# Performance work log

Measured on AMD Instinct MI355X. Metric: run time of the kernel, lower is better.

## Reference

```python
import jax, jax.numpy as jnp
import numpy as np

WS, OWS, NH = 16, 24, 2          # window size, overlap window size (=int(16*0.5)+16), num heads
PAD = (OWS - WS) // 2            # unfold padding = 4


def conv2d(x, w, b):
    kh, kw = w.shape[2], w.shape[3]
    out = jax.lax.conv_general_dilated(x, w, (1, 1), [(kh // 2, kh // 2), (kw // 2, kw // 2)],
                                       dimension_numbers=('NCHW', 'OIHW', 'NCHW'))
    return out + b[None, :, None, None]


def layer_norm(x, g, b, eps=1e-5):
    m = x.mean(-1, keepdims=True)
    v = ((x - m) ** 2).mean(-1, keepdims=True)
    return (x - m) * jax.lax.rsqrt(v + eps) * g + b


def stem(depth, cw1, cb1, cw2, cb2, cw3, cb3, cw4, cb4, in_g, in_b):
    # BasicConv(1->8,k3,relu) -> (8->16,k1,relu) -> (16->16,k3,relu) -> (16->32,k1) -> InstanceNorm2d(32,affine)
    y = jax.nn.relu(conv2d(depth, cw1, cb1))
    y = jax.nn.relu(conv2d(y, cw2, cb2))
    y = jax.nn.relu(conv2d(y, cw3, cb3))
    y = conv2d(y, cw4, cb4)
    m = y.mean((2, 3), keepdims=True)
    v = ((y - m) ** 2).mean((2, 3), keepdims=True)
    return (y - m) * jax.lax.rsqrt(v + 1e-5) * in_g[None, :, None, None] + in_b[None, :, None, None]


def ocab(xq, ykv, rpi, n1g, n1b, wq, bq, wkv, bkv, rpb, wp, bp, n2g, n2b, mw1, mb1, mw2, mb2):
    # Overlapping cross-attention block (HAT-style OCAB, cross variant: q from xq, kv from ykv).
    b, c, h, w = xq.shape
    x = xq.transpose(0, 2, 3, 1)   # b h w c
    y = ykv.transpose(0, 2, 3, 1)
    shortcut = x
    q = layer_norm(x, n1g, n1b) @ wq + bq          # b h w c
    kv = layer_norm(y, n1g, n1b) @ wkv + bkv       # b h w 2c
    nhw, nww = h // WS, w // WS
    # non-overlapping query windows: (b*nw, WS*WS, c)
    qw = q.reshape(b, nhw, WS, nww, WS, c).transpose(0, 1, 3, 2, 4, 5).reshape(b * nhw * nww, WS * WS, c)
    # overlapping kv windows via unfold (patch channel order = (channel, kh, kw), same as torch unfold)
    patches = jax.lax.conv_general_dilated_patches(kv.transpose(0, 3, 1, 2), (OWS, OWS), (WS, WS),
                                                   [(PAD, PAD), (PAD, PAD)])  # b, 2c*OWS*OWS, nhw, nww
    patches = patches.reshape(b, 2, c, OWS * OWS, nhw * nww).transpose(1, 0, 4, 3, 2).reshape(2, b * nhw * nww, OWS * OWS, c)
    k, v = patches[0], patches[1]
    d = c // NH
    qh = qw.reshape(-1, WS * WS, NH, d).transpose(0, 2, 1, 3) * (d ** -0.5)
    kh = k.reshape(-1, OWS * OWS, NH, d).transpose(0, 2, 1, 3)
    vh = v.reshape(-1, OWS * OWS, NH, d).transpose(0, 2, 1, 3)
    attn = jnp.einsum('whqd,whkd->whqk', qh, kh)
    attn = attn + rpb[rpi].transpose(2, 0, 1)[None]  # rel-pos bias -> [1, NH, WS*WS, OWS*OWS]
    attn = jax.nn.softmax(attn, axis=-1)
    out = jnp.einsum('whqk,whkd->whqd', attn, vh).transpose(0, 2, 1, 3).reshape(-1, WS * WS, c)
    # window reverse
    out = out.reshape(b, nhw, nww, WS, WS, c).transpose(0, 1, 3, 2, 4, 5).reshape(b, h, w, c)
    out = out @ wp + bp + shortcut
    out = out + (jax.nn.gelu(layer_norm(out, n2g, n2b) @ mw1 + mb1) @ mw2 + mb2)  # mlp_ratio=2
    return out.transpose(0, 3, 1, 2)


def setup_inputs():
    key = jax.random.key(0)
    ks = jax.random.split(key, 16)
    B, C, H, W = 1, 32, 256, 256
    s = 0.05
    return dict(
        x=jax.random.normal(ks[0], (B, C, H, W), jnp.float32),
        depth=jax.random.normal(ks[1], (B, 1, H, W), jnp.float32),
        rpi=jax.random.randint(ks[2], (WS * WS, OWS * OWS), 0, (WS + OWS - 1) ** 2),
        cw1=jax.random.normal(ks[3], (8, 1, 3, 3)) * s, cb1=jnp.zeros(8),
        cw2=jax.random.normal(ks[4], (16, 8, 1, 1)) * s, cb2=jnp.zeros(16),
        cw3=jax.random.normal(ks[5], (16, 16, 3, 3)) * s, cb3=jnp.zeros(16),
        cw4=jax.random.normal(ks[6], (32, 16, 1, 1)) * s, cb4=jnp.zeros(32),
        in_g=jnp.ones(32), in_b=jnp.zeros(32),
        n1g=jnp.ones(C), n1b=jnp.zeros(C),
        wq=jax.random.normal(ks[7], (C, C)) * s, bq=jnp.zeros(C),
        wkv=jax.random.normal(ks[8], (C, 2 * C)) * s, bkv=jnp.zeros(2 * C),
        rpb=jax.random.normal(ks[9], ((WS + OWS - 1) ** 2, NH)) * 0.02,
        wp=jax.random.normal(ks[10], (C, C)) * s, bp=jnp.zeros(C),
        n2g=jnp.ones(C), n2b=jnp.zeros(C),
        mw1=jax.random.normal(ks[11], (C, 2 * C)) * s, mb1=jnp.zeros(2 * C),
        mw2=jax.random.normal(ks[12], (2 * C, C)) * s, mb2=jnp.zeros(C),
    )


def reference(x, depth, rpi, cw1, cb1, cw2, cb2, cw3, cb3, cw4, cb4, in_g, in_b,
              n1g, n1b, wq, bq, wkv, bkv, rpb, wp, bp, n2g, n2b, mw1, mb1, mw2, mb2):
    f = stem(depth, cw1, cb1, cw2, cb2, cw3, cb3, cw4, cb4, in_g, in_b)
    a = (n1g, n1b, wq, bq, wkv, bkv, rpb, wp, bp, n2g, n2b, mw1, mb1, mw2, mb2)
    out1 = ocab(x, f, rpi, *a)   # shared OCAB weights, called twice with swapped roles
    out2 = ocab(f, x, rpi, *a)
    return out1 + out2 + x
```

## Files before the change

### kernel.cpp

```cpp
#include <hip/hip_runtime.h>
#include <hip/hip_bf16.h>

#define HW 65536
#define KPAD 584

typedef __attribute__((ext_vector_type(8))) short bf8;
typedef __attribute__((ext_vector_type(4))) float f4;

__device__ __forceinline__ unsigned short f2b(float x) {
  unsigned int u = __float_as_uint(x);
  unsigned int r = (u + 0x7fff + ((u >> 16) & 1)) >> 16;
  return (unsigned short)r;
}
__device__ __forceinline__ unsigned int pk2(float lo, float hi) {
  return (__float_as_uint(hi) & 0xffff0000u) | (__float_as_uint(lo) >> 16);
}
__device__ __forceinline__ unsigned int pkrne(float lo, float hi) {
  return ((unsigned int)f2b(hi) << 16) | (unsigned int)f2b(lo);
}
__device__ __forceinline__ float ex2(float x) { return __builtin_amdgcn_exp2f(x); }

__device__ __forceinline__ void stem_front_body(
    int bx, int t, const float* __restrict__ depth,
    const float* __restrict__ cw1, const float* __restrict__ cb1,
    const float* __restrict__ cw2, const float* __restrict__ cb2,
    float* __restrict__ t2) {
  int p = bx * 256 + t;
  int y = p >> 8, x = p & 255;
  float in9[9];
#pragma unroll
  for (int ky = 0; ky < 3; ky++)
#pragma unroll
    for (int kx = 0; kx < 3; kx++) {
      int yy = y + ky - 1, xx = x + kx - 1;
      bool ok = ((unsigned)yy < 256u) && ((unsigned)xx < 256u);
      in9[ky*3+kx] = ok ? depth[yy*256+xx] : 0.f;
    }
  float t1[8];
#pragma unroll
  for (int o = 0; o < 8; o++) {
    float s = cb1[o];
#pragma unroll
    for (int i = 0; i < 9; i++) s += in9[i] * cw1[o*9+i];
    t1[o] = fmaxf(s, 0.f);
  }
#pragma unroll
  for (int o = 0; o < 16; o++) {
    float s = cb2[o];
#pragma unroll
    for (int ci = 0; ci < 8; ci++) s += t1[ci] * cw2[o*8+ci];
    t2[o*HW + p] = fmaxf(s, 0.f);
  }
}

__device__ __forceinline__ void bias_body(
    int bx, int t, const int* __restrict__ rpi,
    const float* __restrict__ rpb, float* __restrict__ biasT) {
  int idx = bx*256 + t;
  int hd = idx / 147456;
  int rem = idx - hd*147456;
  int qt = rem / 9216;
  int r2 = rem - qt*9216;
  int kb = r2 >> 6;
  int q16 = (r2 >> 2) & 15;
  int r = r2 & 3;
  int key = kb*4 + r;
  int qq = qt*16 + q16;
  biasT[idx] = (rpb[rpi[qq*576 + key]*2 + hd] - 8.0f) * 1.44269504f;
}

__device__ __forceinline__ void lnmm48_body(
    int role, int bx, int t,
    float* ws, float* gs, float* bs, float* b2s, float* as_, float* bbs_,
    const float* __restrict__ x, const float* __restrict__ t4,
    const float* __restrict__ part,
    const float* __restrict__ ig, const float* __restrict__ ib,
    const float* __restrict__ n1g, const float* __restrict__ n1b,
    const float* __restrict__ wq, const float* __restrict__ bq,
    const float* __restrict__ wkv, const float* __restrict__ bkv,
    unsigned int* __restrict__ q1, unsigned int* __restrict__ kv1,
    unsigned int* __restrict__ q2, unsigned int* __restrict__ kv2) {
  const float QS = 0.360673503f;
  bool ain = role >= 2;
  int slice = role & 1;
  const float* src = ain ? t4 : x;
  unsigned int* dq  = ain ? q2 : q1;
  unsigned int* dkv = ain ? kv1 : kv2;
  for (int i = t; i < 1536; i += 256) {
    int c = i / 48, j = i - c*48;
    ws[i] = slice ? wkv[c*64 + 16 + j]
                  : (j < 32 ? wq[c*32 + j] : wkv[c*64 + (j - 32)]);
  }
  if (t < 48) b2s[t] = slice ? bkv[16 + t] : (t < 32 ? bq[t] : bkv[t - 32]);
  if (t < 32) {
    gs[t] = n1g[t]; bs[t] = n1b[t];
    if (ain) {
      float s = 0.f, ss = 0.f;
#pragma unroll
      for (int k = 0; k < 16; k++) { s += part[t*16+k]; ss += part[512 + t*16+k]; }
      float m = s * (1.f/65536.f);
      float var = ss * (1.f/65536.f) - m*m;
      float a = rsqrtf(var + 1e-5f) * ig[t];
      as_[t] = a; bbs_[t] = ib[t] - m*a;
    }
  }
  __syncthreads();
  int p = bx*256 + t;
  float v[32]; float s = 0.f;
  if (ain) {
#pragma unroll
    for (int c = 0; c < 32; c++) { v[c] = src[c*HW+p]*as_[c] + bbs_[c]; s += v[c]; }
  } else {
#pragma unroll
    for (int c = 0; c < 32; c++) { v[c] = src[c*HW+p]; s += v[c]; }
  }
  float m = s * 0.03125f;
  float ss = 0.f;
#pragma unroll
  for (int c = 0; c < 32; c++) { float d = v[c]-m; ss += d*d; }
  float rs = rsqrtf(ss*0.03125f + 1e-5f);
  float acc[48];
#pragma unroll
  for (int j = 0; j < 48; j++) acc[j] = b2s[j];
#pragma unroll
  for (int c = 0; c < 32; c++) {
    float ln = (v[c]-m)*rs*gs[c] + bs[c];
    const float4* w4 = (const float4*)&ws[c*48];
#pragma unroll
    for (int j4 = 0; j4 < 12; j4++) {
      float4 w = w4[j4];
      acc[j4*4+0] += ln*w.x; acc[j4*4+1] += ln*w.y;
      acc[j4*4+2] += ln*w.z; acc[j4*4+3] += ln*w.w;
    }
  }
  if (slice == 0) {
#pragma unroll
    for (int j2 = 0; j2 < 16; j2++)
      dq[j2*HW+p] = pkrne(acc[2*j2]*QS, acc[2*j2+1]*QS);
#pragma unroll
    for (int c2 = 0; c2 < 8; c2++)
      dkv[c2*HW+p] = pkrne(acc[32+2*c2], acc[32+2*c2+1]);
  } else {
#pragma unroll
    for (int c2 = 0; c2 < 24; c2++)
      dkv[(8+c2)*HW+p] = pkrne(acc[2*c2], acc[2*c2+1]);
  }
}

__global__ __launch_bounds__(256) void k_misc(
    const float* __restrict__ depth,
    const float* __restrict__ cw1, const float* __restrict__ cb1,
    const float* __restrict__ cw2, const float* __restrict__ cb2,
    float* __restrict__ t2,
    const int* __restrict__ rpi, const float* __restrict__ rpb, float* __restrict__ biasT,
    const float* __restrict__ x, const float* __restrict__ t4,
    const float* __restrict__ part,
    const float* __restrict__ ig, const float* __restrict__ ib,
    const float* __restrict__ n1g, const float* __restrict__ n1b,
    const float* __restrict__ wq, const float* __restrict__ bq,
    const float* __restrict__ wkv, const float* __restrict__ bkv,
    unsigned int* q1, unsigned int* kv1, unsigned int* q2, unsigned int* kv2) {
  __shared__ __align__(16) float ws[1536];
  __shared__ float gs[32], bs[32], b2s[48], as_[32], bbs_[32];
  int id = blockIdx.x, t = threadIdx.x;
  if (id < 256) { stem_front_body(id, t, depth, cw1, cb1, cw2, cb2, t2); return; }
  if (id < 1408) { bias_body(id - 256, t, rpi, rpb, biasT); return; }
  int r = id - 1408;
  lnmm48_body(r >> 8, r & 255, t, ws, gs, bs, b2s, as_, bbs_,
              x, t4, part, ig, ib, n1g, n1b, wq, bq, wkv, bkv, q1, kv1, q2, kv2);
}

__global__ __launch_bounds__(256) void k_lnmmB(
    const float* __restrict__ x, const float* __restrict__ t4,
    const float* __restrict__ part,
    const float* __restrict__ ig, const float* __restrict__ ib,
    const float* __restrict__ n1g, const float* __restrict__ n1b,
    const float* __restrict__ wq, const float* __restrict__ bq,
    const float* __restrict__ wkv, const float* __restrict__ bkv,
    unsigned int* q1, unsigned int* kv1, unsigned int* q2, unsigned int* kv2) {
  __shared__ __align__(16) float ws[1536];
  __shared__ float gs[32], bs[32], b2s[48], as_[32], bbs_[32];
  lnmm48_body(2 + blockIdx.y, blockIdx.x, threadIdx.x, ws, gs, bs, b2s, as_, bbs_,
              x, t4, part, ig, ib, n1g, n1b, wq, bq, wkv, bkv, q1, kv1, q2, kv2);
}

__global__ __launch_bounds__(256) void k_conv3(
    const float* __restrict__ t2, const float* __restrict__ cw3,
    const float* __restrict__ cb3, float* __restrict__ t3) {
  int t = threadIdx.x;
  int p = blockIdx.x*256 + t;
  int og = blockIdx.y;
  int y = p >> 8, x = p & 255;
  float acc[4];
#pragma unroll
  for (int o = 0; o < 4; o++) acc[o] = cb3[og*4+o];
#pragma unroll 1
  for (int tap = 0; tap < 9; tap++) {
    int ky = tap/3 - 1, kx = tap - (tap/3)*3 - 1;
    int yy = y+ky, xx = x+kx;
    bool ok = ((unsigned)yy < 256u) && ((unsigned)xx < 256u);
    int pp = yy*256+xx;
#pragma unroll
    for (int ci = 0; ci < 16; ci++) {
      float v = ok ? t2[ci*HW+pp] : 0.f;
#pragma unroll
      for (int o = 0; o < 4; o++)
        acc[o] += v * cw3[(og*4+o)*144 + ci*9 + tap];
    }
  }
#pragma unroll
  for (int o = 0; o < 4; o++) t3[(og*4+o)*HW+p] = fmaxf(acc[o], 0.f);
}

__global__ __launch_bounds__(256) void k_conv4(
    const float* __restrict__ t3, const float* __restrict__ cw4,
    const float* __restrict__ cb4, float* __restrict__ t4) {
  int t = threadIdx.x;
  int p = blockIdx.x*256 + t;
  int og = blockIdx.y;
  float v[16];
#pragma unroll
  for (int ci = 0; ci < 16; ci++) v[ci] = t3[ci*HW+p];
#pragma unroll
  for (int o = 0; o < 8; o++) {
    int oo = og*8 + o;
    float s = cb4[oo];
#pragma unroll
    for (int ci = 0; ci < 16; ci++) s += v[ci]*cw4[oo*16+ci];
    t4[oo*HW+p] = s;
  }
}

__global__ __launch_bounds__(256) void k_instats1(const float* __restrict__ t4,
                                                  float* __restrict__ part) {
  int c = blockIdx.x >> 4, seg = blockIdx.x & 15;
  const float4* src = (const float4*)(t4 + c*HW + seg*4096);
  float s = 0.f, ss = 0.f;
  for (int i = threadIdx.x; i < 1024; i += 256) {
    float4 v = src[i];
    s  += v.x + v.y + v.z + v.w;
    ss += v.x*v.x + v.y*v.y + v.z*v.z + v.w*v.w;
  }
#pragma unroll
  for (int off = 32; off > 0; off >>= 1) {
    s  += __shfl_down(s, off, 64);
    ss += __shfl_down(ss, off, 64);
  }
  __shared__ float sh[8];
  int wid = threadIdx.x >> 6;
  if ((threadIdx.x & 63) == 0) { sh[wid] = s; sh[4+wid] = ss; }
  __syncthreads();
  if (threadIdx.x == 0) {
    part[blockIdx.x]       = sh[0]+sh[1]+sh[2]+sh[3];
    part[512 + blockIdx.x] = sh[4]+sh[5]+sh[6]+sh[7];
  }
}

__global__ __launch_bounds__(256, 4) void k_attn(
    const unsigned int* __restrict__ qA, const unsigned int* __restrict__ kvA,
    float* __restrict__ aoA,
    const unsigned int* __restrict__ qB, const unsigned int* __restrict__ kvB,
    float* __restrict__ aoB,
    const float* __restrict__ biasT) {
  __shared__ __align__(16) unsigned short Ks[576*16];
  __shared__ __align__(16) unsigned short Vt[16*KPAD];

  const unsigned int* q  = blockIdx.y ? qB  : qA;
  const unsigned int* kv = blockIdx.y ? kvB : kvA;
  float* ao              = blockIdx.y ? aoB : aoA;

  int id = blockIdx.x;
  int lin = ((id & 7) << 6) | (id >> 3);
  int wi = lin >> 1, hd = lin & 1;
  int wy = wi >> 4, wx = wi & 15;
  int t = threadIdx.x;
  int by = wy*16 - 4, bx = wx*16 - 4;
  int krow = hd*8, vrow = 16 + hd*8;

  int wave = t >> 6, lane = t & 63;
  int quad = lane >> 4, l16 = lane & 15;
  const bf8 zero8 = {0,0,0,0,0,0,0,0};

  bf8 qf[4];
#pragma unroll
  for (int qi = 0; qi < 4; qi++) {
    if (quad < 2) {
      int qt = wave*4 + qi;
      int prow = (wy*16 + qt)*256 + wx*16 + l16;
      union { unsigned int u[4]; bf8 v; } Q;
#pragma unroll
      for (int jw = 0; jw < 4; jw++)
        Q.u[jw] = q[(krow + quad*4 + jw)*HW + prow];
      qf[qi] = Q.v;
    } else {
      qf[qi] = zero8;
    }
  }

  for (int e = t; e < 576; e += 256) {
    int dy = e / 24, dx = e - dy*24;
    int yy = by + dy, xx = bx + dx;
    bool ok = ((unsigned)yy < 256u) && ((unsigned)xx < 256u);
    int pp = yy*256 + xx;
    int off = e & 31;
    int ppos = ((off & 12) << 1) + ((off >> 4) << 2) + (off & 3);
    int vcol = (e & ~31) + ppos;
    unsigned int kwd[8];
#pragma unroll
    for (int i = 0; i < 8; i++) kwd[i] = ok ? kv[(krow + i)*HW + pp] : 0u;
    *(uint4*)&Ks[e*16]     = *(const uint4*)&kwd[0];
    *(uint4*)&Ks[e*16 + 8] = *(const uint4*)&kwd[4];
#pragma unroll
    for (int i = 0; i < 8; i++) {
      unsigned int vw = ok ? kv[(vrow + i)*HW + pp] : 0u;
      Vt[(2*i)*KPAD + vcol]   = (unsigned short)vw;
      Vt[(2*i+1)*KPAD + vcol] = (unsigned short)(vw >> 16);
    }
  }
  __syncthreads();

  f4 oacc[4];
  float lr[4];
  const float* bb[4];
#pragma unroll
  for (int qi = 0; qi < 4; qi++) {
    int qt = wave*4 + qi;
    oacc[qi] = (f4){0.f,0.f,0.f,0.f};
    lr[qi] = 0.f;
    bb[qi] = biasT + (hd*16 + qt)*9216 + quad*64 + l16*4;
  }

#pragma unroll 2
  for (int kt2 = 0; kt2 < 18; kt2++) {
    int k0 = kt2 * 32;
    bf8 kf0 = zero8, kf1 = zero8;
    if (quad < 2) {
      kf0 = *(const bf8*)&Ks[(k0 + l16)*16 + quad*8];
      kf1 = *(const bf8*)&Ks[(k0 + 16 + l16)*16 + quad*8];
    }
    bf8 vf = *(const bf8*)&Vt[l16*KPAD + k0 + quad*8];
    __builtin_amdgcn_s_setprio(1);
#pragma unroll
    for (int qi = 0; qi < 4; qi++) {
      f4 b0 = *(const f4*)&bb[qi][k0*16];
      f4 b1 = *(const f4*)&bb[qi][(k0+16)*16];
      f4 s0 = __builtin_amdgcn_mfma_f32_16x16x32_bf16(kf0, qf[qi], b0, 0, 0, 0);
      f4 s1 = __builtin_amdgcn_mfma_f32_16x16x32_bf16(kf1, qf[qi], b1, 0, 0, 0);
      float p0[4], p1[4];
#pragma unroll
      for (int r = 0; r < 4; r++) {
        p0[r] = ex2(s0[r]);
        p1[r] = ex2(s1[r]);
        lr[qi] += p0[r] + p1[r];
      }
      union { unsigned int u[4]; bf8 v; } P;
      P.u[0] = pk2(p0[0], p0[1]); P.u[1] = pk2(p0[2], p0[3]);
      P.u[2] = pk2(p1[0], p1[1]); P.u[3] = pk2(p1[2], p1[3]);
      oacc[qi] = __builtin_amdgcn_mfma_f32_16x16x32_bf16(P.v, vf, oacc[qi], 0, 0, 0);
    }
    __builtin_amdgcn_s_setprio(0);
  }
#pragma unroll
  for (int qi = 0; qi < 4; qi++) {
    lr[qi] += __shfl_xor(lr[qi], 16, 64);
    lr[qi] += __shfl_xor(lr[qi], 32, 64);
  }
#pragma unroll
  for (int qi = 0; qi < 4; qi++) {
    int qt = wave*4 + qi;
#pragma unroll
    for (int r = 0; r < 4; r++) {
      float lv = __shfl(lr[qi], quad*4 + r, 64);
      int qw = qt*16 + quad*4 + r;
      ao[(hd*16 + l16)*HW + (wy*16 + (qw >> 4))*256 + wx*16 + (qw & 15)] = oacc[qi][r] / lv;
    }
  }
}

__global__ __launch_bounds__(256) void k_projmlp(
    const float* __restrict__ ao1, const float* __restrict__ ao2,
    const float* __restrict__ x, const float* __restrict__ t4,
    const float* __restrict__ part,
    const float* __restrict__ ig, const float* __restrict__ ib,
    const float* __restrict__ wp, const float* __restrict__ bp,
    const float* __restrict__ n2g, const float* __restrict__ n2b,
    const float* __restrict__ mw1, const float* __restrict__ mb1,
    const float* __restrict__ mw2, const float* __restrict__ mb2,
    float* __restrict__ o1, float* __restrict__ o2, int obase) {
  int oc = blockIdx.y + obase;
  const float* ao = oc ? ao2 : ao1;
  float* dst      = oc ? o2  : o1;
  __shared__ __align__(16) float wps[1024];
  __shared__ __align__(16) float w1s[2048];
  __shared__ __align__(16) float w2s[2048];
  __shared__ float bps[32], b1s[64], b2s[32], gs[32], bs[32], as[32], bbs[32];
  int t = threadIdx.x;
  for (int i = t; i < 1024; i += 256) wps[i] = wp[i];
  for (int i = t; i < 2048; i += 256) { w1s[i] = mw1[i]; w2s[i] = mw2[i]; }
  if (t < 64) b1s[t] = mb1[t];
  if (t < 32) {
    bps[t] = bp[t]; b2s[t] = mb2[t]; gs[t] = n2g[t]; bs[t] = n2b[t];
    float s = 0.f, ss = 0.f;
#pragma unroll
    for (int k = 0; k < 16; k++) { s += part[t*16+k]; ss += part[512 + t*16+k]; }
    float m = s * (1.f/65536.f);
    float var = ss * (1.f/65536.f) - m*m;
    float a = rsqrtf(var + 1e-5f) * ig[t];
    as[t] = a; bbs[t] = ib[t] - m*a;
  }
  __syncthreads();
  int p = blockIdx.x*256 + t;
  float acc[32];
#pragma unroll
  for (int j = 0; j < 32; j++) acc[j] = bps[j];
#pragma unroll
  for (int c = 0; c < 32; c++) {
    float vc = ao[c*HW+p];
    const float4* w4 = (const float4*)&wps[c*32];
#pragma unroll
    for (int j4 = 0; j4 < 8; j4++) {
      float4 w = w4[j4];
      acc[j4*4+0] += vc*w.x; acc[j4*4+1] += vc*w.y;
      acc[j4*4+2] += vc*w.z; acc[j4*4+3] += vc*w.w;
    }
  }
  if (oc == 0) {
#pragma unroll
    for (int j = 0; j < 32; j++) acc[j] += x[j*HW+p];
  } else {
#pragma unroll
    for (int j = 0; j < 32; j++) acc[j] += t4[j*HW+p]*as[j] + bbs[j];
  }
  float s = 0.f;
#pragma unroll
  for (int j = 0; j < 32; j++) s += acc[j];
  float m = s * 0.03125f;
  float ss = 0.f;
#pragma unroll
  for (int j = 0; j < 32; j++) { float d = acc[j]-m; ss += d*d; }
  float rs = rsqrtf(ss*0.03125f + 1e-5f);
  float r[32];
#pragma unroll
  for (int j = 0; j < 32; j++) r[j] = b2s[j];
#pragma unroll 1
  for (int half = 0; half < 2; half++) {
    float h[32];
#pragma unroll
    for (int k = 0; k < 32; k++) h[k] = b1s[half*32 + k];
#pragma unroll
    for (int c = 0; c < 32; c++) {
      float ln = (acc[c] - m) * rs * gs[c] + bs[c];
      const float4* w4 = (const float4*)&w1s[c*64 + half*32];
#pragma unroll
      for (int k4 = 0; k4 < 8; k4++) {
        float4 w = w4[k4];
        h[k4*4+0] += ln*w.x; h[k4*4+1] += ln*w.y; h[k4*4+2] += ln*w.z; h[k4*4+3] += ln*w.w;
      }
    }
#pragma unroll
    for (int k = 0; k < 32; k++) {
      float xx = h[k];
      float u = 0.7978845608f * (xx + 0.044715f*xx*xx*xx);
      float th = 1.f - 2.f/(1.f + __expf(2.f*u));
      h[k] = 0.5f * xx * (1.f + th);
    }
#pragma unroll
    for (int k = 0; k < 32; k++) {
      float hk = h[k];
      const float4* w4 = (const float4*)&w2s[(half*32 + k)*32];
#pragma unroll
      for (int j4 = 0; j4 < 8; j4++) {
        float4 w = w4[j4];
        r[j4*4+0] += hk*w.x; r[j4*4+1] += hk*w.y; r[j4*4+2] += hk*w.z; r[j4*4+3] += hk*w.w;
      }
    }
  }
#pragma unroll
  for (int j = 0; j < 32; j++) dst[j*HW + p] = acc[j] + r[j];
}

__global__ __launch_bounds__(256) void k_final(
    const float* o1, const float* __restrict__ o2,
    const float* __restrict__ x, float* out) {
  int i = blockIdx.x*256 + threadIdx.x;
  float4 a = ((const float4*)o1)[i];
  float4 b = ((const float4*)o2)[i];
  float4 c = ((const float4*)x)[i];
  float4 r;
  r.x = a.x + b.x + c.x; r.y = a.y + b.y + c.y;
  r.z = a.z + b.z + c.z; r.w = a.w + b.w + c.w;
  ((float4*)out)[i] = r;
}

extern "C" void kernel_launch(void* const* d_in, const int* in_sizes, int n_in,
                              void* d_out, int out_size, void* d_ws, size_t ws_size,
                              hipStream_t stream) {
  const float* x    = (const float*)d_in[0];
  const float* depth= (const float*)d_in[1];
  const int*   rpi  = (const int*)d_in[2];
  const float* cw1  = (const float*)d_in[3],  *cb1 = (const float*)d_in[4];
  const float* cw2  = (const float*)d_in[5],  *cb2 = (const float*)d_in[6];
  const float* cw3  = (const float*)d_in[7],  *cb3 = (const float*)d_in[8];
  const float* cw4  = (const float*)d_in[9],  *cb4 = (const float*)d_in[10];
  const float* in_g = (const float*)d_in[11], *in_b = (const float*)d_in[12];
  const float* n1g  = (const float*)d_in[13], *n1b = (const float*)d_in[14];
  const float* wq   = (const float*)d_in[15], *bq  = (const float*)d_in[16];
  const float* wkv  = (const float*)d_in[17], *bkv = (const float*)d_in[18];
  const float* rpb  = (const float*)d_in[19];
  const float* wp   = (const float*)d_in[20], *bp  = (const float*)d_in[21];
  const float* n2g  = (const float*)d_in[22], *n2b = (const float*)d_in[23];
  const float* mw1  = (const float*)d_in[24], *mb1 = (const float*)d_in[25];
  const float* mw2  = (const float*)d_in[26], *mb2 = (const float*)d_in[27];

  float* W   = (float*)d_ws;
  float* o1  = (float*)d_out;

  float* t4    = W;
  unsigned int* q1  = (unsigned int*)(W + 2097152);
  unsigned int* q2  = (unsigned int*)(W + 3145728);
  unsigned int* kv1 = (unsigned int*)(W + 4194304);
  unsigned int* kv2 = (unsigned int*)(W + 6291456);
  float* ao1   = W + 8388608;
  float* ao2   = W + 10485760;
  float* biasT = W + 12582912;
  float* part  = W + 12877824;
  float* t2 = ao1;
  float* t3 = ao2;
  float* o2 = W + 2097152;

  k_misc   <<<1920, 256, 0, stream>>>(depth, cw1, cb1, cw2, cb2, t2,
                                      rpi, rpb, biasT,
                                      x, t4, part, in_g, in_b, n1g, n1b,
                                      wq, bq, wkv, bkv, q1, kv1, q2, kv2);
  k_conv3  <<<dim3(256,4), 256, 0, stream>>>(t2, cw3, cb3, t3);
  k_conv4  <<<dim3(256,4), 256, 0, stream>>>(t3, cw4, cb4, t4);
  k_instats1<<<512, 256, 0, stream>>>(t4, part);
  k_lnmmB  <<<dim3(256,2), 256, 0, stream>>>(x, t4, part, in_g, in_b, n1g, n1b,
                                             wq, bq, wkv, bkv, q1, kv1, q2, kv2);
  k_attn   <<<dim3(512,2), 256, 0, stream>>>(q1, kv1, ao1, q2, kv2, ao2, biasT);
  k_projmlp<<<dim3(256,2), 256, 0, stream>>>(ao1, ao2, x, t4, part, in_g, in_b,
                                             wp, bp, n2g, n2b, mw1, mb1, mw2, mb2,
                                             o1, o2, 0);
  k_final  <<<2048, 256, 0, stream>>>(o1, o2, x, o1);
}
```

Before: 256.0 us.

## Fuse both OCAB proj/MLP passes and final sum into one kernel; bf16 LN weights

Each thread of k_projmlp now processes both OCAB branches for its pixel at once. The two second-MLP outputs are summed directly into one accumulator and the residuals plus x are added in place, so the o2 intermediate and the k_final kernel are removed. Separately, the LN+QKV projection weights are staged in shared memory as packed bf16 and unpacked on the fly, halving their LDS footprint and load count. The costs are more registers per thread and only 256 blocks for the fused kernel, which may hurt occupancy and latency hiding, and the bf16 weights add rounding error to Q/K/V.

```diff
diff --git a/kernel.cpp b/kernel.cpp
--- a/kernel.cpp
+++ b/kernel.cpp
@@ -18,6 +18,8 @@
 __device__ __forceinline__ unsigned int pkrne(float lo, float hi) {
   return ((unsigned int)f2b(hi) << 16) | (unsigned int)f2b(lo);
 }
+__device__ __forceinline__ float blo(unsigned int u) { return __uint_as_float(u << 16); }
+__device__ __forceinline__ float bhi(unsigned int u) { return __uint_as_float(u & 0xffff0000u); }
 __device__ __forceinline__ float ex2(float x) { return __builtin_amdgcn_exp2f(x); }
 
 __device__ __forceinline__ void stem_front_body(
@@ -71,7 +73,7 @@
 
 __device__ __forceinline__ void lnmm48_body(
     int role, int bx, int t,
-    float* ws, float* gs, float* bs, float* b2s, float* as_, float* bbs_,
+    unsigned int* ws16, float* gs, float* bs, float* b2s, float* as_, float* bbs_,
     const float* __restrict__ x, const float* __restrict__ t4,
     const float* __restrict__ part,
     const float* __restrict__ ig, const float* __restrict__ ib,
@@ -86,10 +88,14 @@
   const float* src = ain ? t4 : x;
   unsigned int* dq  = ain ? q2 : q1;
   unsigned int* dkv = ain ? kv1 : kv2;
-  for (int i = t; i < 1536; i += 256) {
-    int c = i / 48, j = i - c*48;
-    ws[i] = slice ? wkv[c*64 + 16 + j]
-                  : (j < 32 ? wq[c*32 + j] : wkv[c*64 + (j - 32)]);
+  for (int i = t; i < 768; i += 256) {
+    int c = i / 24, jw = i - c*24;
+    int j = jw*2;
+    float a, b;
+    if (slice) { a = wkv[c*64 + 16 + j]; b = wkv[c*64 + 16 + j + 1]; }
+    else if (j < 32) { a = wq[c*32 + j]; b = wq[c*32 + j + 1]; }
+    else { a = wkv[c*64 + (j - 32)]; b = wkv[c*64 + (j - 31)]; }
+    ws16[i] = pkrne(a, b);
   }
   if (t < 48) b2s[t] = slice ? bkv[16 + t] : (t < 32 ? bq[t] : bkv[t - 32]);
   if (t < 32) {
@@ -125,12 +131,14 @@
 #pragma unroll
   for (int c = 0; c < 32; c++) {
     float ln = (v[c]-m)*rs*gs[c] + bs[c];
-    const float4* w4 = (const float4*)&ws[c*48];
-#pragma unroll
-    for (int j4 = 0; j4 < 12; j4++) {
-      float4 w = w4[j4];
-      acc[j4*4+0] += ln*w.x; acc[j4*4+1] += ln*w.y;
-      acc[j4*4+2] += ln*w.z; acc[j4*4+3] += ln*w.w;
+    const uint4* w4 = (const uint4*)&ws16[c*24];
+#pragma unroll
+    for (int q4 = 0; q4 < 6; q4++) {
+      uint4 w = w4[q4];
+      acc[q4*8+0] += ln*blo(w.x); acc[q4*8+1] += ln*bhi(w.x);
+      acc[q4*8+2] += ln*blo(w.y); acc[q4*8+3] += ln*bhi(w.y);
+      acc[q4*8+4] += ln*blo(w.z); acc[q4*8+5] += ln*bhi(w.z);
+      acc[q4*8+6] += ln*blo(w.w); acc[q4*8+7] += ln*bhi(w.w);
     }
   }
   if (slice == 0) {
@@ -160,13 +168,13 @@
     const float* __restrict__ wq, const float* __restrict__ bq,
     const float* __restrict__ wkv, const float* __restrict__ bkv,
     unsigned int* q1, unsigned int* kv1, unsigned int* q2, unsigned int* kv2) {
-  __shared__ __align__(16) float ws[1536];
+  __shared__ __align__(16) unsigned int ws16[768];
   __shared__ float gs[32], bs[32], b2s[48], as_[32], bbs_[32];
   int id = blockIdx.x, t = threadIdx.x;
   if (id < 256) { stem_front_body(id, t, depth, cw1, cb1, cw2, cb2, t2); return; }
   if (id < 1408) { bias_body(id - 256, t, rpi, rpb, biasT); return; }
   int r = id - 1408;
-  lnmm48_body(r >> 8, r & 255, t, ws, gs, bs, b2s, as_, bbs_,
+  lnmm48_body(r >> 8, r & 255, t, ws16, gs, bs, b2s, as_, bbs_,
               x, t4, part, ig, ib, n1g, n1b, wq, bq, wkv, bkv, q1, kv1, q2, kv2);
 }
 
@@ -178,9 +186,9 @@
     const float* __restrict__ wq, const float* __restrict__ bq,
     const float* __restrict__ wkv, const float* __restrict__ bkv,
     unsigned int* q1, unsigned int* kv1, unsigned int* q2, unsigned int* kv2) {
-  __shared__ __align__(16) float ws[1536];
+  __shared__ __align__(16) unsigned int ws16[768];
   __shared__ float gs[32], bs[32], b2s[48], as_[32], bbs_[32];
-  lnmm48_body(2 + blockIdx.y, blockIdx.x, threadIdx.x, ws, gs, bs, b2s, as_, bbs_,
+  lnmm48_body(2 + blockIdx.y, blockIdx.x, threadIdx.x, ws16, gs, bs, b2s, as_, bbs_,
               x, t4, part, ig, ib, n1g, n1b, wq, bq, wkv, bkv, q1, kv1, q2, kv2);
 }
 
@@ -386,14 +394,11 @@
     const float* __restrict__ n2g, const float* __restrict__ n2b,
     const float* __restrict__ mw1, const float* __restrict__ mb1,
     const float* __restrict__ mw2, const float* __restrict__ mb2,
-    float* __restrict__ o1, float* __restrict__ o2, int obase) {
-  int oc = blockIdx.y + obase;
-  const float* ao = oc ? ao2 : ao1;
-  float* dst      = oc ? o2  : o1;
+    float* __restrict__ out) {
   __shared__ __align__(16) float wps[1024];
   __shared__ __align__(16) float w1s[2048];
   __shared__ __align__(16) float w2s[2048];
-  __shared__ float bps[32], b1s[64], b2s[32], gs[32], bs[32], as[32], bbs[32];
+  __shared__ float bps[32], b1s[64], b2s[32], gs[32], bs[32], as_[32], bbs_[32];
   int t = threadIdx.x;
   for (int i = t; i < 1024; i += 256) wps[i] = wp[i];
   for (int i = t; i < 2048; i += 256) { w1s[i] = mw1[i]; w2s[i] = mw2[i]; }
@@ -406,90 +411,93 @@
     float m = s * (1.f/65536.f);
     float var = ss * (1.f/65536.f) - m*m;
     float a = rsqrtf(var + 1e-5f) * ig[t];
-    as[t] = a; bbs[t] = ib[t] - m*a;
+    as_[t] = a; bbs_[t] = ib[t] - m*a;
   }
   __syncthreads();
   int p = blockIdx.x*256 + t;
-  float acc[32];
-#pragma unroll
-  for (int j = 0; j < 32; j++) acc[j] = bps[j];
+
+  float A[32], B[32];
+#pragma unroll
+  for (int j = 0; j < 32; j++) { A[j] = bps[j]; B[j] = bps[j]; }
 #pragma unroll
   for (int c = 0; c < 32; c++) {
-    float vc = ao[c*HW+p];
+    float va = ao1[c*HW+p];
+    float vb = ao2[c*HW+p];
     const float4* w4 = (const float4*)&wps[c*32];
 #pragma unroll
     for (int j4 = 0; j4 < 8; j4++) {
       float4 w = w4[j4];
-      acc[j4*4+0] += vc*w.x; acc[j4*4+1] += vc*w.y;
-      acc[j4*4+2] += vc*w.z; acc[j4*4+3] += vc*w.w;
-    }
-  }
-  if (oc == 0) {
-#pragma unroll
-    for (int j = 0; j < 32; j++) acc[j] += x[j*HW+p];
-  } else {
-#pragma unroll
-    for (int j = 0; j < 32; j++) acc[j] += t4[j*HW+p]*as[j] + bbs[j];
-  }
-  float s = 0.f;
-#pragma unroll
-  for (int j = 0; j < 32; j++) s += acc[j];
-  float m = s * 0.03125f;
-  float ss = 0.f;
-#pragma unroll
-  for (int j = 0; j < 32; j++) { float d = acc[j]-m; ss += d*d; }
-  float rs = rsqrtf(ss*0.03125f + 1e-5f);
-  float r[32];
-#pragma unroll
-  for (int j = 0; j < 32; j++) r[j] = b2s[j];
+      A[j4*4+0] += va*w.x; A[j4*4+1] += va*w.y; A[j4*4+2] += va*w.z; A[j4*4+3] += va*w.w;
+      B[j4*4+0] += vb*w.x; B[j4*4+1] += vb*w.y; B[j4*4+2] += vb*w.z; B[j4*4+3] += vb*w.w;
+    }
+  }
+  float OUT[32];
+#pragma unroll
+  for (int j = 0; j < 32; j++) {
+    float xv = x[j*HW+p];
+    float tv = t4[j*HW+p]*as_[j] + bbs_[j];
+    A[j] += xv; B[j] += tv;
+    OUT[j] = A[j] + B[j] + xv + 2.f*b2s[j];
+  }
+  float sA = 0.f, sB = 0.f;
+#pragma unroll
+  for (int j = 0; j < 32; j++) { sA += A[j]; sB += B[j]; }
+  float mA = sA * 0.03125f, mB = sB * 0.03125f;
+  float ssA = 0.f, ssB = 0.f;
+#pragma unroll
+  for (int j = 0; j < 32; j++) {
+    float dA = A[j]-mA, dB = B[j]-mB;
+    ssA += dA*dA; ssB += dB*dB;
+  }
+  float rsA = rsqrtf(ssA*0.03125f + 1e-5f);
+  float rsB = rsqrtf(ssB*0.03125f + 1e-5f);
+#pragma unroll
+  for (int j = 0; j < 32; j++) {
+    A[j] = (A[j]-mA)*rsA*gs[j] + bs[j];
+    B[j] = (B[j]-mB)*rsB*gs[j] + bs[j];
+  }
 #pragma unroll 1
   for (int half = 0; half < 2; half++) {
-    float h[32];
-#pragma unroll
-    for (int k = 0; k < 32; k++) h[k] = b1s[half*32 + k];
+    float h0[32], h1[32];
+#pragma unroll
+    for (int k = 0; k < 32; k++) { h0[k] = b1s[half*32 + k]; h1[k] = h0[k]; }
 #pragma unroll
     for (int c = 0; c < 32; c++) {
-      float ln = (acc[c] - m) * rs * gs[c] + bs[c];
+      float l0 = A[c], l1 = B[c];
       const float4* w4 = (const float4*)&w1s[c*64 + half*32];
 #pragma unroll
       for (int k4 = 0; k4 < 8; k4++) {
         float4 w = w4[k4];
-        h[k4*4+0] += ln*w.x; h[k4*4+1] += ln*w.y; h[k4*4+2] += ln*w.z; h[k4*4+3] += ln*w.w;
+        h0[k4*4+0] += l0*w.x; h0[k4*4+1] += l0*w.y; h0[k4*4+2] += l0*w.z; h0[k4*4+3] += l0*w.w;
+        h1[k4*4+0] += l1*w.x; h1[k4*4+1] += l1*w.y; h1[k4*4+2] += l1*w.z; h1[k4*4+3] += l1*w.w;
       }
     }
 #pragma unroll
     for (int k = 0; k < 32; k++) {
-      float xx = h[k];
-      float u = 0.7978845608f * (xx + 0.044715f*xx*xx*xx);
-      float th = 1.f - 2.f/(1.f + __expf(2.f*u));
-      h[k] = 0.5f * xx * (1.f + th);
+      float x0 = h0[k], x1 = h1[k];
+      float u0 = 0.7978845608f * (x0 + 0.044715f*x0*x0*x0);
+      float u1 = 0.7978845608f * (x1 + 0.044715f*x1*x1*x1);
+      float th0 = 1.f - 2.f/(1.f + __expf(2.f*u0));
+      float th1 = 1.f - 2.f/(1.f + __expf(2.f*u1));
+      h0[k] = 0.5f * x0 * (1.f + th0);
+      h1[k] = 0.5f * x1 * (1.f + th1);
     }
 #pragma unroll
     for (int k = 0; k < 32; k++) {
-      float hk = h[k];
+      float hk0 = h0[k], hk1 = h1[k];
       const float4* w4 = (const float4*)&w2s[(half*32 + k)*32];
 #pragma unroll
       for (int j4 = 0; j4 < 8; j4++) {
         float4 w = w4[j4];
-        r[j4*4+0] += hk*w.x; r[j4*4+1] += hk*w.y; r[j4*4+2] += hk*w.z; r[j4*4+3] += hk*w.w;
+        OUT[j4*4+0] += hk0*w.x + hk1*w.x;
+        OUT[j4*4+1] += hk0*w.y + hk1*w.y;
+        OUT[j4*4+2] += hk0*w.z + hk1*w.z;
+        OUT[j4*4+3] += hk0*w.w + hk1*w.w;
       }
     }
   }
 #pragma unroll
-  for (int j = 0; j < 32; j++) dst[j*HW + p] = acc[j] + r[j];
-}
-
-__global__ __launch_bounds__(256) void k_final(
-    const float* o1, const float* __restrict__ o2,
-    const float* __restrict__ x, float* out) {
-  int i = blockIdx.x*256 + threadIdx.x;
-  float4 a = ((const float4*)o1)[i];
-  float4 b = ((const float4*)o2)[i];
-  float4 c = ((const float4*)x)[i];
-  float4 r;
-  r.x = a.x + b.x + c.x; r.y = a.y + b.y + c.y;
-  r.z = a.z + b.z + c.z; r.w = a.w + b.w + c.w;
-  ((float4*)out)[i] = r;
+  for (int j = 0; j < 32; j++) out[j*HW + p] = OUT[j];
 }
 
 extern "C" void kernel_launch(void* const* d_in, const int* in_sizes, int n_in,
@@ -526,7 +534,6 @@
   float* part  = W + 12877824;
   float* t2 = ao1;
   float* t3 = ao2;
-  float* o2 = W + 2097152;
 
   k_misc   <<<1920, 256, 0, stream>>>(depth, cw1, cb1, cw2, cb2, t2,
                                       rpi, rpb, biasT,
@@ -538,8 +545,6 @@
   k_lnmmB  <<<dim3(256,2), 256, 0, stream>>>(x, t4, part, in_g, in_b, n1g, n1b,
                                              wq, bq, wkv, bkv, q1, kv1, q2, kv2);
   k_attn   <<<dim3(512,2), 256, 0, stream>>>(q1, kv1, ao1, q2, kv2, ao2, biasT);
-  k_projmlp<<<dim3(256,2), 256, 0, stream>>>(ao1, ao2, x, t4, part, in_g, in_b,
-                                             wp, bp, n2g, n2b, mw1, mb1, mw2, mb2,
-                                             o1, o2, 0);
-  k_final  <<<2048, 256, 0, stream>>>(o1, o2, x, o1);
-}
+  k_projmlp<<<256, 256, 0, stream>>>(ao1, ao2, x, t4, part, in_g, in_b,
+                                     wp, bp, n2g, n2b, mw1, mb1, mw2, mb2, o1);
+}
```

Result: slower. 383.3 us (+49.7%).
